# Kernel tuning notes

Hardware: AMD Instinct MI355X
Metric: run time of the kernel (lower is better)

## Reference

```python
import jax, jax.numpy as jnp
import numpy as np

B, L, D, H = 2, 2048, 1024, 16
DH = D // H
EPS = 1e-5


def setup_inputs() -> dict:
    key = jax.random.key(0)
    ks = jax.random.split(key, 8)
    s = 0.02  # realistic init scale for weights
    # causal mask: True where attention is DISALLOWED (masked_fill semantics)
    mask = jnp.triu(jnp.ones((L, L), dtype=bool), k=1)[None, None]  # [1,1,L,L]
    return {
        "x": jax.random.normal(ks[0], (B, L, D), jnp.float32),
        "mask": mask,
        "ln_g": jnp.ones((D,), jnp.float32),
        "ln_b": jnp.zeros((D,), jnp.float32),
        "Wq": jax.random.normal(ks[1], (D, D), jnp.float32) * s,
        "bq": jnp.zeros((D,), jnp.float32),
        "Wk": jax.random.normal(ks[2], (D, D), jnp.float32) * s,
        "bk": jnp.zeros((D,), jnp.float32),
        "Wv": jax.random.normal(ks[3], (D, D), jnp.float32) * s,
        "bv": jnp.zeros((D,), jnp.float32),
        "Wo": jax.random.normal(ks[4], (D, D), jnp.float32) * s,
        "bo": jnp.zeros((D,), jnp.float32),
    }


def _layernorm(x, g, b):
    mu = jnp.mean(x, axis=-1, keepdims=True)
    var = jnp.var(x, axis=-1, keepdims=True)
    return (x - mu) * jax.lax.rsqrt(var + EPS) * g + b


def reference(x, mask, ln_g, ln_b, Wq, bq, Wk, bk, Wv, bv, Wo, bo):
    b, l, d = x.shape
    h = _layernorm(x, ln_g, ln_b)
    # separate Q/K/V linears, split into heads: [b, H, l, DH]
    q = (h @ Wq + bq).reshape(b, l, H, DH).transpose(0, 2, 1, 3)
    k = (h @ Wk + bk).reshape(b, l, H, DH).transpose(0, 2, 1, 3)
    v = (h @ Wv + bv).reshape(b, l, H, DH).transpose(0, 2, 1, 3)
    scale = jnp.asarray(DH, x.dtype) ** -0.5
    # full L x L score matrix (this is exactly what the torch module does)
    w = jnp.einsum("bhqd,bhkd->bhqk", q, k) * scale
    w = jnp.where(mask, -jnp.inf, w)
    w = jax.nn.softmax(w, axis=-1)
    # dropout layers are identity in eval mode
    o = jnp.einsum("bhqk,bhkd->bhqd", w, v)
    o = o.transpose(0, 2, 1, 3).reshape(b, l, d)
    return o @ Wo + bo
```

## Files before the change

kernel.cpp:

```cpp
#include <hip/hip_runtime.h>
#include <hip/hip_bf16.h>


typedef __bf16  bf16x8 __attribute__((ext_vector_type(8)));
typedef __bf16  bf16x4 __attribute__((ext_vector_type(4)));
typedef float   f32x4  __attribute__((ext_vector_type(4)));

#define MFMA16(a, b, c) __builtin_amdgcn_mfma_f32_16x16x32_bf16(a, b, c, 0, 0, 0)

#define LDT 72

#define QSCALE 0.18033688011112042f

__device__ __forceinline__ void gl_lds16(const void* g, void* l) {
    __builtin_amdgcn_global_load_lds(
        (const __attribute__((address_space(1))) void*)g,
        (__attribute__((address_space(3))) void*)l, 16, 0, 0);
}

__global__ __launch_bounds__(256) void ln_kernel(
    const float* __restrict__ x, const float* __restrict__ g,
    const float* __restrict__ bta, __hip_bfloat16* __restrict__ h)
{
    __shared__ float red[8];
    const int row = blockIdx.x, t = threadIdx.x;
    const float* xr = x + (size_t)row * 1024;
    const float4 xv = *(const float4*)(xr + t * 4);
    float s  = xv.x + xv.y + xv.z + xv.w;
    float ss = xv.x * xv.x + xv.y * xv.y + xv.z * xv.z + xv.w * xv.w;
    #pragma unroll
    for (int off = 32; off > 0; off >>= 1) {
        s  += __shfl_down(s, off);
        ss += __shfl_down(ss, off);
    }
    const int lane = t & 63, wave = t >> 6;
    if (lane == 0) { red[wave] = s; red[4 + wave] = ss; }
    __syncthreads();
    const float S  = red[0] + red[1] + red[2] + red[3];
    const float SS = red[4] + red[5] + red[6] + red[7];
    const float mu   = S * (1.0f / 1024.0f);
    const float var  = SS * (1.0f / 1024.0f) - mu * mu;
    const float rstd = rsqrtf(var + 1e-5f);
    const float4 gv = *(const float4*)(g + t * 4);
    const float4 bv = *(const float4*)(bta + t * 4);
    bf16x4 hv;
    hv[0] = (__bf16)((xv.x - mu) * rstd * gv.x + bv.x);
    hv[1] = (__bf16)((xv.y - mu) * rstd * gv.y + bv.y);
    hv[2] = (__bf16)((xv.z - mu) * rstd * gv.z + bv.z);
    hv[3] = (__bf16)((xv.w - mu) * rstd * gv.w + bv.w);
    *(bf16x4*)(h + (size_t)row * 1024 + t * 4) = hv;
}

__global__ void transpose_cast_kernel(
    const float* __restrict__ Wq, const float* __restrict__ Wk,
    const float* __restrict__ Wv, const float* __restrict__ Wo,
    __hip_bfloat16* __restrict__ tq, __hip_bfloat16* __restrict__ tk,
    __hip_bfloat16* __restrict__ tv, __hip_bfloat16* __restrict__ to_)
{
    __shared__ float t[32][33];
    const int z = blockIdx.z;
    const float* src = (z == 0) ? Wq : (z == 1) ? Wk : (z == 2) ? Wv : Wo;
    __hip_bfloat16* dst = (z == 0) ? tq : (z == 1) ? tk : (z == 2) ? tv : to_;
    const int n0 = blockIdx.x * 32, k0 = blockIdx.y * 32;
    const int tx = threadIdx.x, ty = threadIdx.y;
    t[ty][tx] = src[(size_t)(k0 + ty) * 1024 + n0 + tx];
    __syncthreads();
    dst[(size_t)(n0 + ty) * 1024 + k0 + tx] = __float2bfloat16(t[tx][ty]);
}

__device__ __forceinline__ void gemm_core_1024(
    const __hip_bfloat16* __restrict__ A, const __hip_bfloat16* __restrict__ Bt,
    int m0, int n0, f32x4 (&acc)[4][2])
{
    __shared__ __align__(16) __hip_bfloat16 sA[128 * 32];
    __shared__ __align__(16) __hip_bfloat16 sB[128 * 32];
    const int tid  = threadIdx.x;
    const int wave = tid >> 6, lane = tid & 63;
    const int quad = lane >> 4, l16 = lane & 15;
    const int wm = wave >> 2, wn = wave & 3;

    const f32x4 zero = {0.f, 0.f, 0.f, 0.f};
    #pragma unroll
    for (int i = 0; i < 4; ++i)
        #pragma unroll
        for (int j = 0; j < 2; ++j) acc[i][j] = zero;

    const int r0 = tid >> 2, cc = (tid & 3) << 3;
    const __hip_bfloat16* Ap = A  + (size_t)(m0 + r0) * 1024 + cc;
    const __hip_bfloat16* Bp = Bt + (size_t)(n0 + r0) * 1024 + cc;
    __hip_bfloat16* lA0 = sA + r0 * 32 + cc;
    __hip_bfloat16* lB0 = sB + r0 * 32 + cc;

    for (int k0 = 0; k0 < 1024; k0 += 32) {
        __syncthreads();
        gl_lds16(Ap + k0, lA0);
        gl_lds16(Bp + k0, lB0);
        __syncthreads();
        bf16x8 af[4], bfr[2];
        #pragma unroll
        for (int mt = 0; mt < 4; ++mt)
            af[mt] = *(const bf16x8*)(sA + (wm * 64 + mt * 16 + l16) * 32 + quad * 8);
        #pragma unroll
        for (int nt = 0; nt < 2; ++nt)
            bfr[nt] = *(const bf16x8*)(sB + (wn * 32 + nt * 16 + l16) * 32 + quad * 8);
        #pragma unroll
        for (int mt = 0; mt < 4; ++mt)
            #pragma unroll
            for (int nt = 0; nt < 2; ++nt)
                acc[mt][nt] = MFMA16(af[mt], bfr[nt], acc[mt][nt]);
    }
}

__global__ __launch_bounds__(512) void gemm_qkv_kernel(
    const __hip_bfloat16* __restrict__ h,
    const __hip_bfloat16* __restrict__ wt_base,
    const float* __restrict__ bq, const float* __restrict__ bk,
    const float* __restrict__ bv,
    __hip_bfloat16* __restrict__ qkv_base)
{
    const int z = blockIdx.z;
    const __hip_bfloat16* wt = wt_base + ((size_t)z << 20);
    __hip_bfloat16* outp = qkv_base + ((size_t)z << 22);

    const bool swp = (z == 2);
    const __hip_bfloat16* A  = swp ? wt : h;
    const __hip_bfloat16* Bt = swp ? h  : wt;
    const int m0 = swp ? blockIdx.x * 128 : blockIdx.y * 128;
    const int n0 = swp ? blockIdx.y * 128 : blockIdx.x * 128;

    f32x4 acc[4][2];
    gemm_core_1024(A, Bt, m0, n0, acc);

    const int lane = threadIdx.x & 63, wave = threadIdx.x >> 6;
    const int quad = lane >> 4, l16 = lane & 15;
    const int wm = wave >> 2, wn = wave & 3;

    if (!swp) {
        const float* bias = (z == 0) ? bq : bk;
        const float scale = (z == 0) ? QSCALE : 1.0f;
        #pragma unroll
        for (int mt = 0; mt < 4; ++mt)
            #pragma unroll
            for (int nt = 0; nt < 2; ++nt)
                #pragma unroll
                for (int r = 0; r < 4; ++r) {
                    const int gm = m0 + wm * 64 + mt * 16 + quad * 4 + r;
                    const int gn = n0 + wn * 32 + nt * 16 + l16;
                    const float v = (acc[mt][nt][r] + bias[gn]) * scale;
                    const int b = gm >> 11, l = gm & 2047;
                    const int hh = gn >> 6, dh = gn & 63;
                    outp[(((((size_t)(b * 16 + hh)) << 11) + l) * 64) + dh] = __float2bfloat16(v);
                }
    } else {
        #pragma unroll
        for (int mt = 0; mt < 4; ++mt)
            #pragma unroll
            for (int nt = 0; nt < 2; ++nt)
                #pragma unroll
                for (int r = 0; r < 4; ++r) {
                    const int rr = m0 + wm * 64 + mt * 16 + quad * 4 + r;
                    const int cc = n0 + wn * 32 + nt * 16 + l16;
                    const float v = acc[mt][nt][r] + bv[rr];
                    const int b = cc >> 11, l = cc & 2047;
                    const int hh = rr >> 6, dh = rr & 63;
                    outp[((((size_t)(b * 16 + hh)) * 64 + dh) << 11) + l] = __float2bfloat16(v);
                }
    }
}

__global__ __launch_bounds__(512) void gemm_out_kernel(
    const __hip_bfloat16* __restrict__ o, const __hip_bfloat16* __restrict__ wot,
    const float* __restrict__ bo, float* __restrict__ out)
{
    __shared__ __align__(16) __hip_bfloat16 sA[64 * 32];
    __shared__ __align__(16) __hip_bfloat16 sB[128 * 32];
    const int tid  = threadIdx.x;
    const int wave = tid >> 6, lane = tid & 63;
    const int quad = lane >> 4, l16 = lane & 15;
    const int wm = wave >> 2, wn = wave & 3;
    const int m0 = blockIdx.y * 64, n0 = blockIdx.x * 128;

    const f32x4 zero = {0.f, 0.f, 0.f, 0.f};
    f32x4 acc[2][2];
    #pragma unroll
    for (int i = 0; i < 2; ++i)
        #pragma unroll
        for (int j = 0; j < 2; ++j) acc[i][j] = zero;

    const int r0 = tid >> 2, cc = (tid & 3) << 3;
    const __hip_bfloat16* Ap = o   + (size_t)(m0 + r0) * 1024 + cc;
    const __hip_bfloat16* Bp = wot + (size_t)(n0 + r0) * 1024 + cc;
    __hip_bfloat16* lA0 = sA + r0 * 32 + cc;
    __hip_bfloat16* lB0 = sB + r0 * 32 + cc;

    for (int k0 = 0; k0 < 1024; k0 += 32) {
        __syncthreads();
        if (tid < 256) gl_lds16(Ap + k0, lA0);
        gl_lds16(Bp + k0, lB0);
        __syncthreads();
        bf16x8 af[2], bfr[2];
        #pragma unroll
        for (int mt = 0; mt < 2; ++mt)
            af[mt] = *(const bf16x8*)(sA + (wm * 32 + mt * 16 + l16) * 32 + quad * 8);
        #pragma unroll
        for (int nt = 0; nt < 2; ++nt)
            bfr[nt] = *(const bf16x8*)(sB + (wn * 32 + nt * 16 + l16) * 32 + quad * 8);
        #pragma unroll
        for (int mt = 0; mt < 2; ++mt)
            #pragma unroll
            for (int nt = 0; nt < 2; ++nt)
                acc[mt][nt] = MFMA16(af[mt], bfr[nt], acc[mt][nt]);
    }

    #pragma unroll
    for (int mt = 0; mt < 2; ++mt)
        #pragma unroll
        for (int nt = 0; nt < 2; ++nt)
            #pragma unroll
            for (int r = 0; r < 4; ++r) {
                const int gm = m0 + wm * 32 + mt * 16 + quad * 4 + r;
                const int gn = n0 + wn * 32 + nt * 16 + l16;
                out[(size_t)gm * 1024 + gn] = acc[mt][nt][r] + bo[gn];
            }
}

__global__ __launch_bounds__(512, 4) void attn_kernel(
    const __hip_bfloat16* __restrict__ Q,
    const __hip_bfloat16* __restrict__ Kg,
    const __hip_bfloat16* __restrict__ Vt,
    __hip_bfloat16* __restrict__ O)
{
    __shared__ __align__(16) char smem[55296];
    __hip_bfloat16* sK = (__hip_bfloat16*)smem;
    __hip_bfloat16* sV = (__hip_bfloat16*)(smem + 18432);
    __hip_bfloat16* sP = (__hip_bfloat16*)(smem + 36864);

    const int tid  = threadIdx.x;
    const int wave = tid >> 6, lane = tid & 63;
    const int grp  = wave >> 2, w4 = wave & 3;
    const int quad = lane >> 4, l16 = lane & 15;
    const int bh = blockIdx.x, pi = blockIdx.y;
    const int qtA = 31 - pi, qtB = pi;
    const int q0A = qtA * 64, q0B = qtB * 64;

    const __hip_bfloat16* Qp = Q  + (size_t)bh * 2048 * 64;
    const __hip_bfloat16* Kp = Kg + (size_t)bh * 2048 * 64;
    const __hip_bfloat16* Vp = Vt + (size_t)bh * 64 * 2048;

    const int rA = q0A + w4 * 16 + l16;
    const int rB = q0B + w4 * 16 + l16;
    const bf16x8 aqA0 = *(const bf16x8*)(Qp + (size_t)rA * 64 + quad * 8);
    const bf16x8 aqA1 = *(const bf16x8*)(Qp + (size_t)rA * 64 + 32 + quad * 8);
    const bf16x8 aqB0 = *(const bf16x8*)(Qp + (size_t)rB * 64 + quad * 8);
    const bf16x8 aqB1 = *(const bf16x8*)(Qp + (size_t)rB * 64 + 32 + quad * 8);

    const f32x4 zero = {0.f, 0.f, 0.f, 0.f};
    f32x4 oA[4], oB[4];
    #pragma unroll
    for (int nt = 0; nt < 4; ++nt) { oA[nt] = zero; oB[nt] = zero; }
    float lA = 0.f, lB = 0.f;

    __hip_bfloat16* sPw = sP + (wave * 16) * LDT;
    const int qloc = w4 * 16 + l16;

    const int sg = tid >> 8, tt = tid & 255;

    auto do_tile = [&](const __hip_bfloat16* sKc, const __hip_bfloat16* sVc,
                       const bf16x8& aq0, const bf16x8& aq1,
                       float& l_run, f32x4* oacc, bool diag) {
        f32x4 s[4];
        #pragma unroll
        for (int nt = 0; nt < 4; ++nt) {
            const bf16x8 kf0 = *(const bf16x8*)(sKc + (nt * 16 + l16) * LDT + quad * 8);
            const bf16x8 kf1 = *(const bf16x8*)(sKc + (nt * 16 + l16) * LDT + 32 + quad * 8);
            f32x4 z = zero;
            z = MFMA16(kf0, aq0, z);
            z = MFMA16(kf1, aq1, z);
            s[nt] = z;
        }
        if (diag) {
            #pragma unroll
            for (int nt = 0; nt < 4; ++nt)
                #pragma unroll
                for (int r = 0; r < 4; ++r)
                    if (nt * 16 + quad * 4 + r > qloc) s[nt][r] = -1e30f;
        }
        float rs = 0.f;
        #pragma unroll
        for (int nt = 0; nt < 4; ++nt) {
            bf16x4 pk;
            #pragma unroll
            for (int r = 0; r < 4; ++r) {
                const float p = exp2f(s[nt][r]);
                rs += p;
                pk[r] = (__bf16)p;
            }
            *(bf16x4*)(sPw + l16 * LDT + nt * 16 + quad * 4) = pk;
        }
        rs += __shfl_xor(rs, 16);
        rs += __shfl_xor(rs, 32);
        l_run += rs;
        const bf16x8 ap0 = *(const bf16x8*)(sPw + l16 * LDT + quad * 8);
        const bf16x8 ap1 = *(const bf16x8*)(sPw + l16 * LDT + 32 + quad * 8);
        #pragma unroll
        for (int nt = 0; nt < 4; ++nt) {
            const bf16x8 bv0 = *(const bf16x8*)(sVc + (nt * 16 + l16) * LDT + quad * 8);
            const bf16x8 bv1 = *(const bf16x8*)(sVc + (nt * 16 + l16) * LDT + 32 + quad * 8);
            oacc[nt] = MFMA16(ap0, bv0, oacc[nt]);
            oacc[nt] = MFMA16(ap1, bv1, oacc[nt]);
        }
    };

    for (int r = 0; r < 17; ++r) {
        __syncthreads();
        const int js = 2 * r + sg;
        if (js < 33) {
            const int ktS = (js <= qtA) ? js : js - qtA - 1;
            const int k0 = ktS * 64;
            __hip_bfloat16* sKg = sK + sg * (64 * LDT);
            __hip_bfloat16* sVg = sV + sg * (64 * LDT);
            #pragma unroll
            for (int i = 0; i < 2; ++i) {
                const int chunk = tt + 256 * i, rr = chunk >> 3, cc = (chunk & 7) << 3;
                *(int4*)(sKg + rr * LDT + cc) = *(const int4*)(Kp + (size_t)(k0 + rr) * 64 + cc);
                *(int4*)(sVg + rr * LDT + cc) = *(const int4*)(Vp + (size_t)rr * 2048 + k0 + cc);
            }
        }
        __syncthreads();
        const int j = 2 * r + grp;
        if (j < 33) {
            const bool isA = (j <= qtA);
            const int kt = isA ? j : j - qtA - 1;
            const __hip_bfloat16* sKc = sK + grp * (64 * LDT);
            const __hip_bfloat16* sVc = sV + grp * (64 * LDT);
            if (isA) do_tile(sKc, sVc, aqA0, aqA1, lA, oA, kt == qtA);
            else     do_tile(sKc, sVc, aqB0, aqB1, lB, oB, kt == qtB);
        }
    }

    __syncthreads();
    float* OA1 = (float*)smem;
    float* lA1 = (float*)(smem + 16640);
    float* OB0 = (float*)(smem + 16896);
    float* lB0 = (float*)(smem + 33536);

    if (grp == 1) {
        #pragma unroll
        for (int nt = 0; nt < 4; ++nt)
            #pragma unroll
            for (int r = 0; r < 4; ++r)
                OA1[(w4 * 16 + quad * 4 + r) * 65 + nt * 16 + l16] = oA[nt][r];
        if (quad == 0) lA1[w4 * 16 + l16] = lA;
    } else {
        #pragma unroll
        for (int nt = 0; nt < 4; ++nt)
            #pragma unroll
            for (int r = 0; r < 4; ++r)
                OB0[(w4 * 16 + quad * 4 + r) * 65 + nt * 16 + l16] = oB[nt][r];
        if (quad == 0) lB0[w4 * 16 + l16] = lB;
    }
    __syncthreads();

    const int b = bh >> 4, hh = bh & 15;
    const bool doA = (grp == 0);
    const float* Ox  = doA ? OA1 : OB0;
    const float* lx2 = doA ? lA1 : lB0;
    f32x4* oc = doA ? oA : oB;
    const float lown = doA ? lA : lB;
    const int q0X = doA ? q0A : q0B;

    const float lt = lown + lx2[w4 * 16 + l16];
    float ltr[4];
    #pragma unroll
    for (int r = 0; r < 4; ++r) ltr[r] = 1.0f / __shfl(lt, quad * 4 + r);
    #pragma unroll
    for (int nt = 0; nt < 4; ++nt)
        #pragma unroll
        for (int r = 0; r < 4; ++r) {
            const float oth = Ox[(w4 * 16 + quad * 4 + r) * 65 + nt * 16 + l16];
            const float v = (oc[nt][r] + oth) * ltr[r];
            const int qg = q0X + w4 * 16 + quad * 4 + r;
            const int dh = nt * 16 + l16;
            O[((size_t)b * 2048 + qg) * 1024 + hh * 64 + dh] = __float2bfloat16(v);
        }
}

extern "C" void kernel_launch(void* const* d_in, const int* in_sizes, int n_in,
                              void* d_out, int out_size, void* d_ws, size_t ws_size,
                              hipStream_t stream) {
    const float* x    = (const float*)d_in[0];
    const float* ln_g = (const float*)d_in[2];
    const float* ln_b = (const float*)d_in[3];
    const float* Wq = (const float*)d_in[4];  const float* bq = (const float*)d_in[5];
    const float* Wk = (const float*)d_in[6];  const float* bk = (const float*)d_in[7];
    const float* Wv = (const float*)d_in[8];  const float* bv = (const float*)d_in[9];
    const float* Wo = (const float*)d_in[10]; const float* bo = (const float*)d_in[11];
    float* out = (float*)d_out;

    __hip_bfloat16* ws = (__hip_bfloat16*)d_ws;
    const size_t M1 = 1024 * 1024;
    __hip_bfloat16* h   = ws;
    __hip_bfloat16* wqt = ws + 4 * M1;
    __hip_bfloat16* wot = ws + 7 * M1;
    __hip_bfloat16* q   = ws + 8 * M1;
    __hip_bfloat16* k   = ws + 12 * M1;
    __hip_bfloat16* vt  = ws + 16 * M1;
    __hip_bfloat16* o   = h;

    ln_kernel<<<4096, 256, 0, stream>>>(x, ln_g, ln_b, h);
    transpose_cast_kernel<<<dim3(32, 32, 4), dim3(32, 32), 0, stream>>>(
        Wq, Wk, Wv, Wo, wqt, wqt + M1, wqt + 2 * M1, wot);
    gemm_qkv_kernel<<<dim3(8, 32, 3), 512, 0, stream>>>(h, wqt, bq, bk, bv, q);
    attn_kernel<<<dim3(32, 16), 512, 0, stream>>>(q, k, vt, o);
    gemm_out_kernel<<<dim3(8, 64), 512, 0, stream>>>(o, wot, bo, out);
}
```

Before: 206.5 us.

## Switch attention kernel to 32x32x16 MFMA tiles with shared P staging

Rewrites the attention inner loop to use 32x32x16 bf16 MFMA instructions. Each wave now computes a 32-key by 32-query score block, with P written to a per-group shared tile and consumed after an extra block barrier. Q fragments are held in registers in the new layout, and the epilogue merges partial O and row sums across waves and groups. The aim is fewer MFMA issues and fewer LDS fragment loads per tile, at the cost of an additional __syncthreads per iteration and a more involved final reduction.

```diff
diff --git a/kernel.cpp b/kernel.cpp
--- a/kernel.cpp
+++ b/kernel.cpp
@@ -5,10 +5,13 @@
 typedef __bf16  bf16x8 __attribute__((ext_vector_type(8)));
 typedef __bf16  bf16x4 __attribute__((ext_vector_type(4)));
 typedef float   f32x4  __attribute__((ext_vector_type(4)));
+typedef float   f32x16 __attribute__((ext_vector_type(16)));
 
 #define MFMA16(a, b, c) __builtin_amdgcn_mfma_f32_16x16x32_bf16(a, b, c, 0, 0, 0)
+#define MFMA32(a, b, c) __builtin_amdgcn_mfma_f32_32x32x16_bf16(a, b, c, 0, 0, 0)
 
 #define LDT 72
+#define LDP 72
 
 #define QSCALE 0.18033688011112042f
 
@@ -238,7 +241,8 @@
     const int tid  = threadIdx.x;
     const int wave = tid >> 6, lane = tid & 63;
     const int grp  = wave >> 2, w4 = wave & 3;
-    const int quad = lane >> 4, l16 = lane & 15;
+    const int wk = w4 >> 1, wq = w4 & 1;
+    const int q5 = lane & 31, hi = lane >> 5;
     const int bh = blockIdx.x, pi = blockIdx.y;
     const int qtA = 31 - pi, qtB = pi;
     const int q0A = qtA * 64, q0B = qtB * 64;
@@ -247,69 +251,24 @@
     const __hip_bfloat16* Kp = Kg + (size_t)bh * 2048 * 64;
     const __hip_bfloat16* Vp = Vt + (size_t)bh * 64 * 2048;
 
-    const int rA = q0A + w4 * 16 + l16;
-    const int rB = q0B + w4 * 16 + l16;
-    const bf16x8 aqA0 = *(const bf16x8*)(Qp + (size_t)rA * 64 + quad * 8);
-    const bf16x8 aqA1 = *(const bf16x8*)(Qp + (size_t)rA * 64 + 32 + quad * 8);
-    const bf16x8 aqB0 = *(const bf16x8*)(Qp + (size_t)rB * 64 + quad * 8);
-    const bf16x8 aqB1 = *(const bf16x8*)(Qp + (size_t)rB * 64 + 32 + quad * 8);
-
-    const f32x4 zero = {0.f, 0.f, 0.f, 0.f};
-    f32x4 oA[4], oB[4];
-    #pragma unroll
-    for (int nt = 0; nt < 4; ++nt) { oA[nt] = zero; oB[nt] = zero; }
+    bf16x8 QfA[4], QfB[4];
+    #pragma unroll
+    for (int ks = 0; ks < 4; ++ks) {
+        QfA[ks] = *(const bf16x8*)(Qp + (size_t)(q0A + wq * 32 + q5) * 64 + ks * 16 + hi * 8);
+        QfB[ks] = *(const bf16x8*)(Qp + (size_t)(q0B + wq * 32 + q5) * 64 + ks * 16 + hi * 8);
+    }
+
+    f32x16 oA, oB;
+    #pragma unroll
+    for (int r = 0; r < 16; ++r) { oA[r] = 0.f; oB[r] = 0.f; }
     float lA = 0.f, lB = 0.f;
 
-    __hip_bfloat16* sPw = sP + (wave * 16) * LDT;
-    const int qloc = w4 * 16 + l16;
+    const __hip_bfloat16* sKg = sK + grp * (64 * LDT);
+    const __hip_bfloat16* sVg = sV + grp * (64 * LDT);
+    __hip_bfloat16*       sPg = sP + grp * (64 * LDP);
+    const int qloc = wq * 32 + q5;
 
     const int sg = tid >> 8, tt = tid & 255;
-
-    auto do_tile = [&](const __hip_bfloat16* sKc, const __hip_bfloat16* sVc,
-                       const bf16x8& aq0, const bf16x8& aq1,
-                       float& l_run, f32x4* oacc, bool diag) {
-        f32x4 s[4];
-        #pragma unroll
-        for (int nt = 0; nt < 4; ++nt) {
-            const bf16x8 kf0 = *(const bf16x8*)(sKc + (nt * 16 + l16) * LDT + quad * 8);
-            const bf16x8 kf1 = *(const bf16x8*)(sKc + (nt * 16 + l16) * LDT + 32 + quad * 8);
-            f32x4 z = zero;
-            z = MFMA16(kf0, aq0, z);
-            z = MFMA16(kf1, aq1, z);
-            s[nt] = z;
-        }
-        if (diag) {
-            #pragma unroll
-            for (int nt = 0; nt < 4; ++nt)
-                #pragma unroll
-                for (int r = 0; r < 4; ++r)
-                    if (nt * 16 + quad * 4 + r > qloc) s[nt][r] = -1e30f;
-        }
-        float rs = 0.f;
-        #pragma unroll
-        for (int nt = 0; nt < 4; ++nt) {
-            bf16x4 pk;
-            #pragma unroll
-            for (int r = 0; r < 4; ++r) {
-                const float p = exp2f(s[nt][r]);
-                rs += p;
-                pk[r] = (__bf16)p;
-            }
-            *(bf16x4*)(sPw + l16 * LDT + nt * 16 + quad * 4) = pk;
-        }
-        rs += __shfl_xor(rs, 16);
-        rs += __shfl_xor(rs, 32);
-        l_run += rs;
-        const bf16x8 ap0 = *(const bf16x8*)(sPw + l16 * LDT + quad * 8);
-        const bf16x8 ap1 = *(const bf16x8*)(sPw + l16 * LDT + 32 + quad * 8);
-        #pragma unroll
-        for (int nt = 0; nt < 4; ++nt) {
-            const bf16x8 bv0 = *(const bf16x8*)(sVc + (nt * 16 + l16) * LDT + quad * 8);
-            const bf16x8 bv1 = *(const bf16x8*)(sVc + (nt * 16 + l16) * LDT + 32 + quad * 8);
-            oacc[nt] = MFMA16(ap0, bv0, oacc[nt]);
-            oacc[nt] = MFMA16(ap1, bv1, oacc[nt]);
-        }
-    };
 
     for (int r = 0; r < 17; ++r) {
         __syncthreads();
@@ -317,72 +276,116 @@
         if (js < 33) {
             const int ktS = (js <= qtA) ? js : js - qtA - 1;
             const int k0 = ktS * 64;
-            __hip_bfloat16* sKg = sK + sg * (64 * LDT);
-            __hip_bfloat16* sVg = sV + sg * (64 * LDT);
+            __hip_bfloat16* dK = sK + sg * (64 * LDT);
+            __hip_bfloat16* dV = sV + sg * (64 * LDT);
             #pragma unroll
             for (int i = 0; i < 2; ++i) {
                 const int chunk = tt + 256 * i, rr = chunk >> 3, cc = (chunk & 7) << 3;
-                *(int4*)(sKg + rr * LDT + cc) = *(const int4*)(Kp + (size_t)(k0 + rr) * 64 + cc);
-                *(int4*)(sVg + rr * LDT + cc) = *(const int4*)(Vp + (size_t)rr * 2048 + k0 + cc);
+                *(int4*)(dK + rr * LDT + cc) = *(const int4*)(Kp + (size_t)(k0 + rr) * 64 + cc);
+                *(int4*)(dV + rr * LDT + cc) = *(const int4*)(Vp + (size_t)rr * 2048 + k0 + cc);
             }
         }
         __syncthreads();
+
         const int j = 2 * r + grp;
-        if (j < 33) {
-            const bool isA = (j <= qtA);
+        const bool act = (j < 33);
+        bool isA = true;
+        if (act) {
+            isA = (j <= qtA);
             const int kt = isA ? j : j - qtA - 1;
-            const __hip_bfloat16* sKc = sK + grp * (64 * LDT);
-            const __hip_bfloat16* sVc = sV + grp * (64 * LDT);
-            if (isA) do_tile(sKc, sVc, aqA0, aqA1, lA, oA, kt == qtA);
-            else     do_tile(sKc, sVc, aqB0, aqB1, lB, oB, kt == qtB);
+            const bool diag = isA ? (kt == qtA) : (kt == qtB);
+            const bf16x8* Qf = isA ? QfA : QfB;
+
+            f32x16 s;
+            #pragma unroll
+            for (int i = 0; i < 16; ++i) s[i] = 0.f;
+            #pragma unroll
+            for (int ks = 0; ks < 4; ++ks) {
+                const bf16x8 kf = *(const bf16x8*)(sKg + (wk * 32 + q5) * LDT + ks * 16 + hi * 8);
+                s = MFMA32(kf, Qf[ks], s);
+            }
+            if (diag) {
+                #pragma unroll
+                for (int i = 0; i < 16; ++i) {
+                    const int krow = wk * 32 + (i & 3) + 8 * (i >> 2) + 4 * hi;
+                    if (krow > qloc) s[i] = -1e30f;
+                }
+            }
+            float rs = 0.f;
+            #pragma unroll
+            for (int rb = 0; rb < 4; ++rb) {
+                bf16x4 pk;
+                #pragma unroll
+                for (int i = 0; i < 4; ++i) {
+                    const float p = exp2f(s[rb * 4 + i]);
+                    rs += p;
+                    pk[i] = (__bf16)p;
+                }
+                *(bf16x4*)(sPg + (wq * 32 + q5) * LDP + wk * 32 + 8 * rb + 4 * hi) = pk;
+            }
+            rs += __shfl_xor(rs, 32);
+            if (isA) lA += rs; else lB += rs;
         }
+        __syncthreads();
+
+        if (act) {
+            f32x16& oacc = isA ? oA : oB;
+            #pragma unroll
+            for (int ks = 0; ks < 4; ++ks) {
+                const bf16x8 vf = *(const bf16x8*)(sVg + (wk * 32 + q5) * LDT + ks * 16 + hi * 8);
+                const bf16x8 pf = *(const bf16x8*)(sPg + (wq * 32 + q5) * LDP + ks * 16 + hi * 8);
+                oacc = MFMA32(vf, pf, oacc);
+            }
+        }
     }
 
     __syncthreads();
-    float* OA1 = (float*)smem;
-    float* lA1 = (float*)(smem + 16640);
-    float* OB0 = (float*)(smem + 16896);
-    float* lB0 = (float*)(smem + 33536);
+    float* Oscr = (float*)smem;
+    float* lscr = (float*)(smem + 33280);
 
     if (grp == 1) {
         #pragma unroll
-        for (int nt = 0; nt < 4; ++nt)
-            #pragma unroll
-            for (int r = 0; r < 4; ++r)
-                OA1[(w4 * 16 + quad * 4 + r) * 65 + nt * 16 + l16] = oA[nt][r];
-        if (quad == 0) lA1[w4 * 16 + l16] = lA;
-    } else {
-        #pragma unroll
-        for (int nt = 0; nt < 4; ++nt)
-            #pragma unroll
-            for (int r = 0; r < 4; ++r)
-                OB0[(w4 * 16 + quad * 4 + r) * 65 + nt * 16 + l16] = oB[nt][r];
-        if (quad == 0) lB0[w4 * 16 + l16] = lB;
+        for (int t2 = 0; t2 < 2; ++t2) {
+            const f32x16& oc = t2 ? oB : oA;
+            float* base = Oscr + t2 * 4160;
+            #pragma unroll
+            for (int i = 0; i < 16; ++i) {
+                const int dh = wk * 32 + (i & 3) + 8 * (i >> 2) + 4 * hi;
+                base[dh * 65 + wq * 32 + q5] = oc[i];
+            }
+        }
+    }
+    if (hi == 0) {
+        lscr[((0 * 2 + grp) * 2 + wk) * 64 + wq * 32 + q5] = lA;
+        lscr[((1 * 2 + grp) * 2 + wk) * 64 + wq * 32 + q5] = lB;
     }
     __syncthreads();
 
-    const int b = bh >> 4, hh = bh & 15;
-    const bool doA = (grp == 0);
-    const float* Ox  = doA ? OA1 : OB0;
-    const float* lx2 = doA ? lA1 : lB0;
-    f32x4* oc = doA ? oA : oB;
-    const float lown = doA ? lA : lB;
-    const int q0X = doA ? q0A : q0B;
-
-    const float lt = lown + lx2[w4 * 16 + l16];
-    float ltr[4];
-    #pragma unroll
-    for (int r = 0; r < 4; ++r) ltr[r] = 1.0f / __shfl(lt, quad * 4 + r);
-    #pragma unroll
-    for (int nt = 0; nt < 4; ++nt)
-        #pragma unroll
-        for (int r = 0; r < 4; ++r) {
-            const float oth = Ox[(w4 * 16 + quad * 4 + r) * 65 + nt * 16 + l16];
-            const float v = (oc[nt][r] + oth) * ltr[r];
-            const int qg = q0X + w4 * 16 + quad * 4 + r;
-            const int dh = nt * 16 + l16;
-            O[((size_t)b * 2048 + qg) * 1024 + hh * 64 + dh] = __float2bfloat16(v);
+    if (grp == 0) {
+        const int b = bh >> 4, hh = bh & 15;
+        #pragma unroll
+        for (int t2 = 0; t2 < 2; ++t2) {
+            const f32x16& oc = t2 ? oB : oA;
+            const float* base = Oscr + t2 * 4160;
+            const int q0X = t2 ? q0B : q0A;
+            const int qq = wq * 32 + q5;
+            const float lt = lscr[((t2 * 2 + 0) * 2 + 0) * 64 + qq]
+                           + lscr[((t2 * 2 + 0) * 2 + 1) * 64 + qq]
+                           + lscr[((t2 * 2 + 1) * 2 + 0) * 64 + qq]
+                           + lscr[((t2 * 2 + 1) * 2 + 1) * 64 + qq];
+            const float linv = 1.0f / lt;
+            __hip_bfloat16* Orow = O + ((size_t)b * 2048 + q0X + qq) * 1024 + hh * 64;
+            #pragma unroll
+            for (int rb = 0; rb < 4; ++rb) {
+                const int dh0 = wk * 32 + 8 * rb + 4 * hi;
+                bf16x4 ov;
+                #pragma unroll
+                for (int i = 0; i < 4; ++i)
+                    ov[i] = (__bf16)((oc[rb * 4 + i] + base[(dh0 + i) * 65 + qq]) * linv);
+                *(bf16x4*)(Orow + dh0) = ov;
+            }
         }
+    }
 }
 
 extern "C" void kernel_launch(void* const* d_in, const int* in_sizes, int n_in,
```

Result: slower. 263.0 us (+27.4%).
